# Kernel tuning notes

Measured on AMD Instinct MI355X. Metric: run time of the kernel, lower is better.

The kernel has to match this reference:

```python
import jax, jax.numpy as jnp
import numpy as np

EPS = 1e-8
NS = 1e9  # nanoseconds per second


def qmult(a, b):
    aw, ax, ay, az = a[..., 0], a[..., 1], a[..., 2], a[..., 3]
    bw, bx, by, bz = b[..., 0], b[..., 1], b[..., 2], b[..., 3]
    return jnp.stack([
        aw * bw - ax * bx - ay * by - az * bz,
        aw * bx + ax * bw + ay * bz - az * by,
        aw * by - ax * bz + ay * bw + az * bx,
        aw * bz + ax * by - ay * bx + az * bw,
    ], axis=-1)


def qinv(q):
    # unit-quaternion inverse == conjugate
    return q * jnp.array([1.0, -1.0, -1.0, -1.0], dtype=q.dtype)


def qexp(v):
    # log-quaternion (..., 3) -> unit quaternion (..., 4)
    n = jnp.maximum(jnp.linalg.norm(v, axis=-1, keepdims=True), EPS)
    return jnp.concatenate([jnp.cos(n), jnp.sin(n) / n * v], axis=-1)


def qlog(q):
    # unit quaternion (..., 4) -> log-quaternion (..., 3)
    n = jnp.maximum(jnp.linalg.norm(q[..., 1:], axis=-1, keepdims=True), EPS)
    return q[..., 1:] * jnp.arccos(jnp.clip(q[..., :1], -1.0, 1.0)) / n


def rotate_vec(v, q):
    # rotate vector v (..., 3) by quaternion q (..., 4)
    vq = jnp.concatenate([jnp.zeros_like(v[..., :1]), v], axis=-1)
    return qmult(qmult(q, vq), qinv(q))[..., 1:]


def l1(a, b):
    return jnp.mean(jnp.abs(a - b))


def setup_inputs() -> dict:
    key = jax.random.key(0)
    k1, k2, k3 = jax.random.split(key, 3)
    N, T = 2048, 1024
    pred = jax.random.normal(k1, (N, T, 6), dtype=jnp.float32)
    targ = jax.random.normal(k2, (N, T, 6), dtype=jnp.float32)
    imu = jax.random.normal(k3, (N, T, 10), dtype=jnp.float32)
    ts = jnp.broadcast_to(jnp.arange(T, dtype=jnp.float32) * 5e6, (N, T))
    imu = imu.at[..., 9].set(ts)
    z = jnp.zeros((1,), dtype=jnp.float32)
    return {"pred": pred, "targ": targ, "imu": imu,
            "sax": z, "saq": z, "srx": z, "srq": z}


def reference(pred, targ, imu, sax, saq, srx, srq):
    # ---- absolute pose loss ----
    abs_loss = (jnp.exp(-sax) * l1(pred[..., :3], targ[..., :3]) + sax
                + jnp.exp(-saq) * l1(pred[..., 3:], targ[..., 3:]) + saq)

    # ---- simple VOs: consecutive differences (N, T-1, 6) ----
    pred_vos = pred[:, 1:] - pred[:, :-1]
    targ_vos = targ[:, 1:] - targ[:, :-1]

    # ---- true relative poses from targ (calc_vos) ----
    q0 = qexp(targ[:, :-1, 3:])            # (N, T-1, 4)
    q1 = qexp(targ[:, 1:, 3:])
    q0i = qinv(q0)
    targ_imu_q = qlog(qmult(q0i, q1))      # (N, T-1, 3) rotation part of calc_vos

    # ---- IMU integration (vectorized over the original N x T python loop) ----
    ts = imu[..., 9]
    dt = ((ts[:, 1:] - ts[:, :-1]) / NS)[..., None]   # (N, T-1, 1) seconds
    accel = imu[:, :-1, 0:3]
    vel = imu[:, :-1, 3:6]
    ang_vel = imu[:, :-1, 6:9]
    imu_trans = vel * dt + 0.5 * accel * dt * dt       # (N, T-1, 3)

    wnorm = jnp.maximum(jnp.linalg.norm(ang_vel, axis=-1, keepdims=True), EPS)
    theta = wnorm * dt                                  # rotation angle over dt
    dq = jnp.concatenate([jnp.cos(0.5 * theta),
                          (ang_vel / wnorm) * jnp.sin(0.5 * theta)], axis=-1)
    new_q = jax.lax.stop_gradient(qmult(q0, dq))        # numpy round-trip in torch detaches
    imu_ori_shift = qlog(qmult(q0i, new_q))             # (N, T-1, 3)

    # ---- relative (VO) loss ----
    vo_loss = (jnp.exp(-srx) * l1(pred_vos[..., :3], targ_vos[..., :3]) + srx
               + jnp.exp(-srq) * l1(pred_vos[..., 3:], targ_vos[..., 3:]) + srq)

    # ---- IMU loss ----
    imu_loss = (jnp.exp(-srx) * l1(pred_vos[..., :3], imu_trans) + srx
                + jnp.exp(-srq) * l1(targ_imu_q, imu_ori_shift) + srq)

    return abs_loss + vo_loss + imu_loss   # shape (1,)
```

## Files before the change

### kernel.cpp

```cpp
#include <hip/hip_runtime.h>
#include <math.h>

#define NN 2048
#define TT 1024
#define EPSF 1e-8f
#define BLOCK 256
#define HALF 512
#define NBLK (NN * 2)

struct Quat { float w, x, y, z; };

__device__ inline float fsqrt_f(float x) { return __builtin_amdgcn_sqrtf(x); }
__device__ inline float frcp_f(float x)  { return __builtin_amdgcn_rcpf(x); }

__device__ inline float acos_fast(float x) {
    float ax = fabsf(x);
    float p = fmaf(ax, -0.0187293f, 0.0742610f);
    p = fmaf(ax, p, -0.2121144f);
    p = fmaf(ax, p, 1.5707288f);
    float r = fsqrt_f(1.0f - ax) * p;
    return x >= 0.0f ? r : 3.14159274f - r;
}

__device__ inline Quat qmul(const Quat a, const Quat b) {
    Quat r;
    r.w = a.w * b.w - a.x * b.x - a.y * b.y - a.z * b.z;
    r.x = a.w * b.x + a.x * b.w + a.y * b.z - a.z * b.y;
    r.y = a.w * b.y - a.x * b.z + a.y * b.w + a.z * b.x;
    r.z = a.w * b.z + a.x * b.y - a.y * b.x + a.z * b.w;
    return r;
}

__device__ inline Quat qconj(const Quat q) {
    Quat r; r.w = q.w; r.x = -q.x; r.y = -q.y; r.z = -q.z; return r;
}

__device__ inline Quat qexp3(float vx, float vy, float vz) {
    float ss = fmaf(vx, vx, fmaf(vy, vy, vz * vz));
    float n = fmaxf(fsqrt_f(ss), EPSF);
    float s = __sinf(n) * frcp_f(n);
    Quat r; r.w = __cosf(n); r.x = s * vx; r.y = s * vy; r.z = s * vz;
    return r;
}

__device__ inline void qlog3(const Quat q, float& ox, float& oy, float& oz) {
    float ss = fmaf(q.x, q.x, fmaf(q.y, q.y, q.z * q.z));
    float n = fmaxf(fsqrt_f(ss), EPSF);
    float c = fminf(fmaxf(q.w, -1.0f), 1.0f);
    float s = acos_fast(c) * frcp_f(n);
    ox = q.x * s; oy = q.y * s; oz = q.z * s;
}

__device__ inline float waveReduceF(float v) {
    #pragma unroll
    for (int o = 32; o > 0; o >>= 1) v += __shfl_down(v, o);
    return v;
}

__device__ inline double waveReduceD(double v) {
    #pragma unroll
    for (int o = 32; o > 0; o >>= 1) v += __shfl_down(v, o);
    return v;
}

__device__ inline void pair_terms(
    const float* pa, const float* pb, const float* ga, const float* gb,
    const Quat qR, const Quat qN,
    float a0, float a1, float a2, float v0, float v1, float v2,
    float w0, float w1, float w2, float ts0, float ts1,
    float& s2, float& s3, float& s4, float& s5)
{
    float pv0 = pb[0] - pa[0], pv1 = pb[1] - pa[1], pv2 = pb[2] - pa[2];
    float pv3 = pb[3] - pa[3], pv4 = pb[4] - pa[4], pv5 = pb[5] - pa[5];
    float tv0 = gb[0] - ga[0], tv1 = gb[1] - ga[1], tv2 = gb[2] - ga[2];
    float tv3 = gb[3] - ga[3], tv4 = gb[4] - ga[4], tv5 = gb[5] - ga[5];

    s2 += fabsf(pv0 - tv0) + fabsf(pv1 - tv1) + fabsf(pv2 - tv2);
    s3 += fabsf(pv3 - tv3) + fabsf(pv4 - tv4) + fabsf(pv5 - tv5);

    Quat r01 = qmul(qconj(qR), qN);
    float tq0, tq1, tq2;
    qlog3(r01, tq0, tq1, tq2);

    float dt = (ts1 - ts0) * 1e-9f;
    float hdt2 = 0.5f * dt * dt;
    float it0 = fmaf(v0, dt, a0 * hdt2);
    float it1 = fmaf(v1, dt, a1 * hdt2);
    float it2 = fmaf(v2, dt, a2 * hdt2);
    s4 += fabsf(pv0 - it0) + fabsf(pv1 - it1) + fabsf(pv2 - it2);

    float kk = 0.5f * dt;
    s5 += fabsf(tq0 - kk * w0) + fabsf(tq1 - kk * w1) + fabsf(tq2 - kk * w2);
}

__global__ __launch_bounds__(BLOCK) void loss_main(
    const float* __restrict__ pred, const float* __restrict__ targ,
    const float* __restrict__ imu, float* __restrict__ partial)
{
    __shared__ __align__(16) float sp[HALF * 6];
    __shared__ __align__(16) float sg[HALF * 6];
    __shared__ __align__(16) float si[HALF * 10];
    __shared__ float nbr[13];
    __shared__ float red[4][6];

    const int tid = threadIdx.x;
    const int bid = blockIdx.x;
    const int n = bid >> 1, h = bid & 1;

    const float* pbase = pred + ((size_t)n * TT + (size_t)h * HALF) * 6;
    const float* gbase = targ + ((size_t)n * TT + (size_t)h * HALF) * 6;
    const float* ibase = imu  + ((size_t)n * TT + (size_t)h * HALF) * 10;

    if (h == 0) {
        if (tid < 6)        nbr[tid] = pbase[HALF * 6 + tid];
        else if (tid < 12)  nbr[tid] = gbase[HALF * 6 + (tid - 6)];
        else if (tid == 12) nbr[12]  = ibase[HALF * 10 + 9];
    }

    const float4* pg4 = reinterpret_cast<const float4*>(pbase);
    const float4* gg4 = reinterpret_cast<const float4*>(gbase);
    const float4* ig4 = reinterpret_cast<const float4*>(ibase);
    float4* sp4 = reinterpret_cast<float4*>(sp);
    float4* sg4 = reinterpret_cast<float4*>(sg);
    float4* si4 = reinterpret_cast<float4*>(si);
    #pragma unroll
    for (int k = 0; k < 3; ++k) sp4[tid + k * BLOCK] = pg4[tid + k * BLOCK];
    #pragma unroll
    for (int k = 0; k < 3; ++k) sg4[tid + k * BLOCK] = gg4[tid + k * BLOCK];
    #pragma unroll
    for (int k = 0; k < 5; ++k) si4[tid + k * BLOCK] = ig4[tid + k * BLOCK];

    __syncthreads();

    float s0 = 0.f, s1 = 0.f, s2 = 0.f, s3 = 0.f, s4 = 0.f, s5 = 0.f;

    const float2* P = reinterpret_cast<const float2*>(sp + tid * 12);
    const float2* G = reinterpret_cast<const float2*>(sg + tid * 12);
    const float2* I = reinterpret_cast<const float2*>(si + tid * 20);

    float2 P0 = P[0], P1 = P[1], P2 = P[2], P3 = P[3], P4 = P[4], P5 = P[5];
    float2 G0 = G[0], G1 = G[1], G2 = G[2], G3 = G[3], G4 = G[4], G5 = G[5];
    float2 I0 = I[0], I1 = I[1], I2 = I[2], I3 = I[3], I4 = I[4];
    float2 I5 = I[5], I6 = I[6], I7 = I[7], I8 = I[8], I9 = I[9];

    float pA[6] = {P0.x, P0.y, P1.x, P1.y, P2.x, P2.y};
    float pB[6] = {P3.x, P3.y, P4.x, P4.y, P5.x, P5.y};
    float gA[6] = {G0.x, G0.y, G1.x, G1.y, G2.x, G2.y};
    float gB[6] = {G3.x, G3.y, G4.x, G4.y, G5.x, G5.y};

    s0 += fabsf(pA[0]-gA[0]) + fabsf(pA[1]-gA[1]) + fabsf(pA[2]-gA[2])
        + fabsf(pB[0]-gB[0]) + fabsf(pB[1]-gB[1]) + fabsf(pB[2]-gB[2]);
    s1 += fabsf(pA[3]-gA[3]) + fabsf(pA[4]-gA[4]) + fabsf(pA[5]-gA[5])
        + fabsf(pB[3]-gB[3]) + fabsf(pB[4]-gB[4]) + fabsf(pB[5]-gB[5]);

    Quat qA = qexp3(gA[3], gA[4], gA[5]);
    Quat qB = qexp3(gB[3], gB[4], gB[5]);

    float tsA = I4.y, tsB = I9.y;

    pair_terms(pA, pB, gA, gB, qA, qB,
               I0.x, I0.y, I1.x,
               I1.y, I2.x, I2.y,
               I3.x, I3.y, I4.x,
               tsA, tsB, s2, s3, s4, s5);

    const bool lastPair = (tid == BLOCK - 1);
    if (!(h == 1 && lastPair)) {
        float pC[6], gC[6], tsC;
        if (!lastPair) {
            const float2* Pn = reinterpret_cast<const float2*>(sp + tid * 12 + 12);
            const float2* Gn = reinterpret_cast<const float2*>(sg + tid * 12 + 12);
            float2 a = Pn[0], b = Pn[1], c = Pn[2];
            float2 d = Gn[0], e = Gn[1], f = Gn[2];
            pC[0]=a.x; pC[1]=a.y; pC[2]=b.x; pC[3]=b.y; pC[4]=c.x; pC[5]=c.y;
            gC[0]=d.x; gC[1]=d.y; gC[2]=e.x; gC[3]=e.y; gC[4]=f.x; gC[5]=f.y;
            tsC = si[tid * 20 + 29];
        } else {
            pC[0]=nbr[0]; pC[1]=nbr[1]; pC[2]=nbr[2]; pC[3]=nbr[3]; pC[4]=nbr[4]; pC[5]=nbr[5];
            gC[0]=nbr[6]; gC[1]=nbr[7]; gC[2]=nbr[8]; gC[3]=nbr[9]; gC[4]=nbr[10]; gC[5]=nbr[11];
            tsC = nbr[12];
        }
        Quat qC = qexp3(gC[3], gC[4], gC[5]);
        pair_terms(pB, pC, gB, gC, qB, qC,
                   I5.x, I5.y, I6.x,
                   I6.y, I7.x, I7.y,
                   I8.x, I8.y, I9.x,
                   tsB, tsC, s2, s3, s4, s5);
    }

    s0 = waveReduceF(s0); s1 = waveReduceF(s1); s2 = waveReduceF(s2);
    s3 = waveReduceF(s3); s4 = waveReduceF(s4); s5 = waveReduceF(s5);

    const int lane = tid & 63;
    const int wid  = tid >> 6;
    if (lane == 0) {
        red[wid][0] = s0; red[wid][1] = s1; red[wid][2] = s2;
        red[wid][3] = s3; red[wid][4] = s4; red[wid][5] = s5;
    }
    __syncthreads();
    if (tid < 6) {
        const int c = tid;
        partial[(size_t)bid * 6 + c] = red[0][c] + red[1][c] + red[2][c] + red[3][c];
    }
}

__global__ __launch_bounds__(256) void loss_finalize(
    const float* __restrict__ partial,
    const float* __restrict__ sax, const float* __restrict__ saq,
    const float* __restrict__ srx, const float* __restrict__ srq,
    float* __restrict__ out)
{
    double t0 = 0, t1 = 0, t2 = 0, t3 = 0, t4 = 0, t5 = 0;
    for (int r = threadIdx.x; r < NBLK; r += 256) {
        const float* p = partial + (size_t)r * 6;
        t0 += p[0]; t1 += p[1]; t2 += p[2];
        t3 += p[3]; t4 += p[4]; t5 += p[5];
    }
    t0 = waveReduceD(t0); t1 = waveReduceD(t1); t2 = waveReduceD(t2);
    t3 = waveReduceD(t3); t4 = waveReduceD(t4); t5 = waveReduceD(t5);

    __shared__ double red[4][6];
    const int lane = threadIdx.x & 63;
    const int wid  = threadIdx.x >> 6;
    if (lane == 0) {
        red[wid][0] = t0; red[wid][1] = t1; red[wid][2] = t2;
        red[wid][3] = t3; red[wid][4] = t4; red[wid][5] = t5;
    }
    __syncthreads();
    if (threadIdx.x == 0) {
        double a0 = 0, a1 = 0, a2 = 0, a3 = 0, a4 = 0, a5 = 0;
        #pragma unroll
        for (int w = 0; w < 4; ++w) {
            a0 += red[w][0]; a1 += red[w][1]; a2 += red[w][2];
            a3 += red[w][3]; a4 += red[w][4]; a5 += red[w][5];
        }
        const double inv_abs = 1.0 / ((double)NN * TT * 3);
        const double inv_vo  = 1.0 / ((double)NN * (TT - 1) * 3);
        float A = (float)(a0 * inv_abs);
        float B = (float)(a1 * inv_abs);
        float C = (float)(a2 * inv_vo);
        float D = (float)(a3 * inv_vo);
        float E = (float)(a4 * inv_vo);
        float F = (float)(a5 * inv_vo);
        float sx = sax[0], sq = saq[0], rx = srx[0], rq = srq[0];
        out[0] = expf(-sx) * A + sx + expf(-sq) * B + sq
               + expf(-rx) * (C + E) + 2.0f * rx
               + expf(-rq) * (D + F) + 2.0f * rq;
    }
}

extern "C" void kernel_launch(void* const* d_in, const int* in_sizes, int n_in,
                              void* d_out, int out_size, void* d_ws, size_t ws_size,
                              hipStream_t stream) {
    const float* pred = (const float*)d_in[0];
    const float* targ = (const float*)d_in[1];
    const float* imu  = (const float*)d_in[2];
    const float* sax  = (const float*)d_in[3];
    const float* saq  = (const float*)d_in[4];
    const float* srx  = (const float*)d_in[5];
    const float* srq  = (const float*)d_in[6];
    float* out = (float*)d_out;
    float* partial = (float*)d_ws;

    loss_main<<<NBLK, BLOCK, 0, stream>>>(pred, targ, imu, partial);
    loss_finalize<<<1, 256, 0, stream>>>(partial, sax, saq, srx, srq, out);
}
```

Before: 209.7 us.

## Replace LDS staging with direct global loads and wave-shuffle neighbor exchange

Drops the shared-memory staging of pred/targ/imu rows. Each lane now loads its pair of timesteps directly from global memory as float4 vectors, and the next pair's pose and quaternion come from a lane shuffle. Waves overlap by one lane (63 active pairs per wave), so the grid is sized by pairs rather than by sequence halves. This removes LDS traffic and the block barrier, at the cost of non-contiguous per-lane float4 loads, one idle lane per wave, and slightly more blocks.

```diff
diff --git a/kernel.cpp b/kernel.cpp
--- a/kernel.cpp
+++ b/kernel.cpp
@@ -4,9 +4,12 @@
 #define NN 2048
 #define TT 1024
 #define EPSF 1e-8f
+
+#define NPAIR (NN * TT / 2)
 #define BLOCK 256
-#define HALF 512
-#define NBLK (NN * 2)
+#define WPB   (BLOCK / 64)
+#define NWAVE ((NPAIR + 62) / 63)
+#define NBLK  ((NWAVE + WPB - 1) / WPB)
 
 struct Quat { float w, x, y, z; };
 
@@ -97,102 +100,71 @@
     const float* __restrict__ pred, const float* __restrict__ targ,
     const float* __restrict__ imu, float* __restrict__ partial)
 {
-    __shared__ __align__(16) float sp[HALF * 6];
-    __shared__ __align__(16) float sg[HALF * 6];
-    __shared__ __align__(16) float si[HALF * 10];
-    __shared__ float nbr[13];
-    __shared__ float red[4][6];
-
-    const int tid = threadIdx.x;
-    const int bid = blockIdx.x;
-    const int n = bid >> 1, h = bid & 1;
-
-    const float* pbase = pred + ((size_t)n * TT + (size_t)h * HALF) * 6;
-    const float* gbase = targ + ((size_t)n * TT + (size_t)h * HALF) * 6;
-    const float* ibase = imu  + ((size_t)n * TT + (size_t)h * HALF) * 10;
-
-    if (h == 0) {
-        if (tid < 6)        nbr[tid] = pbase[HALF * 6 + tid];
-        else if (tid < 12)  nbr[tid] = gbase[HALF * 6 + (tid - 6)];
-        else if (tid == 12) nbr[12]  = ibase[HALF * 10 + 9];
-    }
-
-    const float4* pg4 = reinterpret_cast<const float4*>(pbase);
-    const float4* gg4 = reinterpret_cast<const float4*>(gbase);
-    const float4* ig4 = reinterpret_cast<const float4*>(ibase);
-    float4* sp4 = reinterpret_cast<float4*>(sp);
-    float4* sg4 = reinterpret_cast<float4*>(sg);
-    float4* si4 = reinterpret_cast<float4*>(si);
-    #pragma unroll
-    for (int k = 0; k < 3; ++k) sp4[tid + k * BLOCK] = pg4[tid + k * BLOCK];
-    #pragma unroll
-    for (int k = 0; k < 3; ++k) sg4[tid + k * BLOCK] = gg4[tid + k * BLOCK];
-    #pragma unroll
-    for (int k = 0; k < 5; ++k) si4[tid + k * BLOCK] = ig4[tid + k * BLOCK];
-
-    __syncthreads();
-
-    float s0 = 0.f, s1 = 0.f, s2 = 0.f, s3 = 0.f, s4 = 0.f, s5 = 0.f;
-
-    const float2* P = reinterpret_cast<const float2*>(sp + tid * 12);
-    const float2* G = reinterpret_cast<const float2*>(sg + tid * 12);
-    const float2* I = reinterpret_cast<const float2*>(si + tid * 20);
-
-    float2 P0 = P[0], P1 = P[1], P2 = P[2], P3 = P[3], P4 = P[4], P5 = P[5];
-    float2 G0 = G[0], G1 = G[1], G2 = G[2], G3 = G[3], G4 = G[4], G5 = G[5];
-    float2 I0 = I[0], I1 = I[1], I2 = I[2], I3 = I[3], I4 = I[4];
-    float2 I5 = I[5], I6 = I[6], I7 = I[7], I8 = I[8], I9 = I[9];
-
-    float pA[6] = {P0.x, P0.y, P1.x, P1.y, P2.x, P2.y};
-    float pB[6] = {P3.x, P3.y, P4.x, P4.y, P5.x, P5.y};
-    float gA[6] = {G0.x, G0.y, G1.x, G1.y, G2.x, G2.y};
-    float gB[6] = {G3.x, G3.y, G4.x, G4.y, G5.x, G5.y};
-
-    s0 += fabsf(pA[0]-gA[0]) + fabsf(pA[1]-gA[1]) + fabsf(pA[2]-gA[2])
-        + fabsf(pB[0]-gB[0]) + fabsf(pB[1]-gB[1]) + fabsf(pB[2]-gB[2]);
-    s1 += fabsf(pA[3]-gA[3]) + fabsf(pA[4]-gA[4]) + fabsf(pA[5]-gA[5])
-        + fabsf(pB[3]-gB[3]) + fabsf(pB[4]-gB[4]) + fabsf(pB[5]-gB[5]);
+    const int tid  = threadIdx.x;
+    const int lane = tid & 63;
+    const int wid  = tid >> 6;
+
+    const long wave = (long)blockIdx.x * WPB + wid;
+    const long u    = wave * 63 + lane;
+    const bool valid  = (u < NPAIR);
+    const bool active = (lane < 63) && valid;
+    const long uc = valid ? u : (NPAIR - 1);
+
+    const float4* p4 = reinterpret_cast<const float4*>(pred) + uc * 3;
+    const float4* g4 = reinterpret_cast<const float4*>(targ) + uc * 3;
+    const float4* i4 = reinterpret_cast<const float4*>(imu)  + uc * 5;
+
+    float4 P0 = p4[0], P1 = p4[1], P2 = p4[2];
+    float4 G0 = g4[0], G1 = g4[1], G2 = g4[2];
+    float4 I0 = i4[0], I1 = i4[1], I2 = i4[2], I3 = i4[3], I4 = i4[4];
+
+    float pA[6] = {P0.x, P0.y, P0.z, P0.w, P1.x, P1.y};
+    float pB[6] = {P1.z, P1.w, P2.x, P2.y, P2.z, P2.w};
+    float gA[6] = {G0.x, G0.y, G0.z, G0.w, G1.x, G1.y};
+    float gB[6] = {G1.z, G1.w, G2.x, G2.y, G2.z, G2.w};
 
     Quat qA = qexp3(gA[3], gA[4], gA[5]);
     Quat qB = qexp3(gB[3], gB[4], gB[5]);
-
-    float tsA = I4.y, tsB = I9.y;
-
-    pair_terms(pA, pB, gA, gB, qA, qB,
-               I0.x, I0.y, I1.x,
-               I1.y, I2.x, I2.y,
-               I3.x, I3.y, I4.x,
-               tsA, tsB, s2, s3, s4, s5);
-
-    const bool lastPair = (tid == BLOCK - 1);
-    if (!(h == 1 && lastPair)) {
-        float pC[6], gC[6], tsC;
-        if (!lastPair) {
-            const float2* Pn = reinterpret_cast<const float2*>(sp + tid * 12 + 12);
-            const float2* Gn = reinterpret_cast<const float2*>(sg + tid * 12 + 12);
-            float2 a = Pn[0], b = Pn[1], c = Pn[2];
-            float2 d = Gn[0], e = Gn[1], f = Gn[2];
-            pC[0]=a.x; pC[1]=a.y; pC[2]=b.x; pC[3]=b.y; pC[4]=c.x; pC[5]=c.y;
-            gC[0]=d.x; gC[1]=d.y; gC[2]=e.x; gC[3]=e.y; gC[4]=f.x; gC[5]=f.y;
-            tsC = si[tid * 20 + 29];
-        } else {
-            pC[0]=nbr[0]; pC[1]=nbr[1]; pC[2]=nbr[2]; pC[3]=nbr[3]; pC[4]=nbr[4]; pC[5]=nbr[5];
-            gC[0]=nbr[6]; gC[1]=nbr[7]; gC[2]=nbr[8]; gC[3]=nbr[9]; gC[4]=nbr[10]; gC[5]=nbr[11];
-            tsC = nbr[12];
+    float tsA = I2.y, tsB = I4.w;
+
+    float pC[6], gC[6];
+    #pragma unroll
+    for (int j = 0; j < 6; ++j) {
+        pC[j] = __shfl_down(pA[j], 1);
+        gC[j] = __shfl_down(gA[j], 1);
+    }
+    float tsC = __shfl_down(tsA, 1);
+    Quat qC;
+    qC.w = __shfl_down(qA.w, 1); qC.x = __shfl_down(qA.x, 1);
+    qC.y = __shfl_down(qA.y, 1); qC.z = __shfl_down(qA.z, 1);
+
+    float s0 = 0.f, s1 = 0.f, s2 = 0.f, s3 = 0.f, s4 = 0.f, s5 = 0.f;
+
+    if (active) {
+        s0 += fabsf(pA[0]-gA[0]) + fabsf(pA[1]-gA[1]) + fabsf(pA[2]-gA[2])
+            + fabsf(pB[0]-gB[0]) + fabsf(pB[1]-gB[1]) + fabsf(pB[2]-gB[2]);
+        s1 += fabsf(pA[3]-gA[3]) + fabsf(pA[4]-gA[4]) + fabsf(pA[5]-gA[5])
+            + fabsf(pB[3]-gB[3]) + fabsf(pB[4]-gB[4]) + fabsf(pB[5]-gB[5]);
+
+        pair_terms(pA, pB, gA, gB, qA, qB,
+                   I0.x, I0.y, I0.z,
+                   I0.w, I1.x, I1.y,
+                   I1.z, I1.w, I2.x,
+                   tsA, tsB, s2, s3, s4, s5);
+
+        if ((u & 511) != 511) {
+            pair_terms(pB, pC, gB, gC, qB, qC,
+                       I2.z, I2.w, I3.x,
+                       I3.y, I3.z, I3.w,
+                       I4.x, I4.y, I4.z,
+                       tsB, tsC, s2, s3, s4, s5);
         }
-        Quat qC = qexp3(gC[3], gC[4], gC[5]);
-        pair_terms(pB, pC, gB, gC, qB, qC,
-                   I5.x, I5.y, I6.x,
-                   I6.y, I7.x, I7.y,
-                   I8.x, I8.y, I9.x,
-                   tsB, tsC, s2, s3, s4, s5);
     }
 
     s0 = waveReduceF(s0); s1 = waveReduceF(s1); s2 = waveReduceF(s2);
     s3 = waveReduceF(s3); s4 = waveReduceF(s4); s5 = waveReduceF(s5);
 
-    const int lane = tid & 63;
-    const int wid  = tid >> 6;
+    __shared__ float red[WPB][6];
     if (lane == 0) {
         red[wid][0] = s0; red[wid][1] = s1; red[wid][2] = s2;
         red[wid][3] = s3; red[wid][4] = s4; red[wid][5] = s5;
@@ -200,7 +172,7 @@
     __syncthreads();
     if (tid < 6) {
         const int c = tid;
-        partial[(size_t)bid * 6 + c] = red[0][c] + red[1][c] + red[2][c] + red[3][c];
+        partial[(size_t)blockIdx.x * 6 + c] = red[0][c] + red[1][c] + red[2][c] + red[3][c];
     }
 }
 
```

Measured after the change: 206.4 us. No clear change (-1.6%).
